# Optimization experiments

Hardware: AMD Instinct MI355X
Metric: run time of the kernel (lower is better)

Reference implementation:

```python
import jax, jax.numpy as jnp
import numpy as np

N = 16384      # nodes (radar cells x batched graphs)
H = 128        # n_hidden
N_ENV = 7
N_IN = N_ENV + 2 + 1  # env + coords + density = 10
T_CTX = 24
HORIZON = 40
T = T_CTX + HORIZON


def setup_inputs() -> dict:
    key = jax.random.key(0)
    ks = jax.random.split(key, 40)

    def w(k, shape, fan_in):
        return jax.random.normal(k, shape, jnp.float32) * np.float32(1.0 / np.sqrt(fan_in))

    inp = {}
    inp["x"] = jax.random.normal(ks[0], (N, T), jnp.float32)
    inp["coords"] = jax.random.normal(ks[1], (N, 2), jnp.float32)
    inp["env"] = jax.random.normal(ks[2], (N, N_ENV, T), jnp.float32)
    # --- encoder params ---
    inp["enc_W_in"] = w(ks[3], (H, N_IN), N_IN)           # Linear(n_in->H), no bias
    inp["enc_Wih0"] = w(ks[4], (4 * H, H), H)
    inp["enc_Whh0"] = w(ks[5], (4 * H, H), H)
    inp["enc_bih0"] = jnp.zeros((4 * H,), jnp.float32)
    inp["enc_bhh0"] = jnp.zeros((4 * H,), jnp.float32)
    inp["enc_Wih1"] = w(ks[6], (4 * H, H), H)
    inp["enc_Whh1"] = w(ks[7], (4 * H, H), H)
    inp["enc_bih1"] = jnp.zeros((4 * H,), jnp.float32)
    inp["enc_bhh1"] = jnp.zeros((4 * H,), jnp.float32)
    # --- NodeLSTM params ---
    inp["node_W_in"] = w(ks[8], (H, N_IN), N_IN)          # Linear(n_in->H), no bias
    inp["in_Wih"] = w(ks[9], (4 * H, 2 * H), 2 * H)       # lstm_in takes [inputs, enc_state]
    inp["in_Whh"] = w(ks[10], (4 * H, H), H)
    inp["in_bih"] = jnp.zeros((4 * H,), jnp.float32)
    inp["in_bhh"] = jnp.zeros((4 * H,), jnp.float32)
    inp["l1_Wih"] = w(ks[11], (4 * H, H), H)
    inp["l1_Whh"] = w(ks[12], (4 * H, H), H)
    inp["l1_bih"] = jnp.zeros((4 * H,), jnp.float32)
    inp["l1_bhh"] = jnp.zeros((4 * H,), jnp.float32)
    # hidden2in / hidden2out heads: Linear(H,H) -> ReLU -> Linear(H,1)
    inp["h2in_W1"] = w(ks[13], (H, H), H)
    inp["h2in_b1"] = jnp.zeros((H,), jnp.float32)
    inp["h2in_W2"] = w(ks[14], (1, H), H)
    inp["h2in_b2"] = jnp.zeros((1,), jnp.float32)
    inp["h2out_W1"] = w(ks[15], (H, H), H)
    inp["h2out_b1"] = jnp.zeros((H,), jnp.float32)
    inp["h2out_W2"] = w(ks[16], (1, H), H)
    inp["h2out_b2"] = jnp.zeros((1,), jnp.float32)
    return inp


def _lstm_cell(xin, h, c, Wih, Whh, bih, bhh):
    # torch.nn.LSTMCell semantics; gate order i, f, g, o
    gates = xin @ Wih.T + h @ Whh.T + (bih + bhh)
    i, f, g, o = jnp.split(gates, 4, axis=1)
    c_new = jax.nn.sigmoid(f) * c + jax.nn.sigmoid(i) * jnp.tanh(g)
    h_new = jax.nn.sigmoid(o) * jnp.tanh(c_new)
    return h_new, c_new


def reference(x, coords, env,
              enc_W_in, enc_Wih0, enc_Whh0, enc_bih0, enc_bhh0,
              enc_Wih1, enc_Whh1, enc_bih1, enc_bhh1,
              node_W_in, in_Wih, in_Whh, in_bih, in_bhh,
              l1_Wih, l1_Whh, l1_bih, l1_bhh,
              h2in_W1, h2in_b1, h2in_W2, h2in_b2,
              h2out_W1, h2out_b1, h2out_W2, h2out_b2):
    n = x.shape[0]
    z = jnp.zeros((n, H), x.dtype)

    # ---------- encoder: scan over T_CTX context steps ----------
    def enc_step(carry, xs):
        h0, c0, h1, c1 = carry
        xt, et = xs  # [N], [N, N_ENV]
        inp = jnp.concatenate([xt[:, None], coords, et], axis=1) @ enc_W_in.T
        h0, c0 = _lstm_cell(inp, h0, c0, enc_Wih0, enc_Whh0, enc_bih0, enc_bhh0)
        h1, c1 = _lstm_cell(h0, h1, c1, enc_Wih1, enc_Whh1, enc_bih1, enc_bhh1)
        return (h0, c0, h1, c1), None

    enc_xs = (x[:, :T_CTX].T, jnp.moveaxis(env[:, :, :T_CTX], 2, 0))
    (h0, c0, h1, c1), _ = jax.lax.scan(enc_step, (z, z, z, z), enc_xs)
    enc_state = h1  # h[-1] captured at setup_states, fixed over the horizon

    def head(hid, W1, b1, W2, b2):
        return jax.nn.sigmoid(jax.nn.relu(hid @ W1.T + b1) @ W2.T + b2)

    # ---------- decoder: scan over HORIZON forecast steps ----------
    def dec_step(carry, et):
        xc, h0, c0, h1, c1 = carry
        inp = jnp.concatenate([xc, coords, et], axis=1) @ node_W_in.T
        inp = jnp.concatenate([inp, enc_state], axis=1)  # [N, 2H]
        h0, c0 = _lstm_cell(inp, h0, c0, in_Wih, in_Whh, in_bih, in_bhh)
        h1, c1 = _lstm_cell(h0, h1, c1, l1_Wih, l1_Whh, l1_bih, l1_bhh)
        x_in = head(h1, h2in_W1, h2in_b1, h2in_W2, h2in_b2)
        x_out = head(h1, h2out_W1, h2out_b1, h2out_W2, h2out_b2)
        xn = xc + x_in - x_out * xc  # source/sink update, [N, 1]
        return (xn, h0, c0, h1, c1), xn

    x0 = x[:, T_CTX - 1][:, None]
    dec_xs = jnp.moveaxis(env[:, :, T_CTX:T_CTX + HORIZON], 2, 0)
    _, ys = jax.lax.scan(dec_step, (x0, h0, c0, h1, c1), dec_xs)  # [HORIZON, N, 1]
    return jnp.transpose(ys[..., 0], (1, 0))  # [N, HORIZON]
```

## Files before the change

### kernel.cpp

```cpp
#include <hip/hip_runtime.h>
#include <hip/hip_bf16.h>
#include <cstdint>
#include <cstddef>

typedef __bf16 bf16_t;
typedef bf16_t bf16x8 __attribute__((ext_vector_type(8)));
typedef bf16_t bf16x4 __attribute__((ext_vector_type(4)));
typedef float  f32x4  __attribute__((ext_vector_type(4)));

#define TT    64
#define T_CTX 24
#define HOR   40
#define SA    264
#define NTH   512

#define MFMA __builtin_amdgcn_mfma_f32_16x16x32_bf16

#define O_PKE   16
#define O_PKD   (O_PKE + 262144)
#define O_PKX   (O_PKD + 294912)
#define O_BIAS  (O_PKX + 131072)
#define O_HEADP (O_BIAS + 2048)
#define O_WINE  (O_HEADP + 512)
#define O_WINN  (O_WINE + 1536)
#define O_B2    (O_WINN + 1536)

struct Ptrs { const void* q[29]; };

__device__ __forceinline__ float sigm(float x) {
  return __builtin_amdgcn_rcpf(1.f + __expf(-x));
}
__device__ __forceinline__ float tanh_(float x) {
  return 1.f - 2.f * __builtin_amdgcn_rcpf(1.f + __expf(2.f * x));
}
__device__ __forceinline__ unsigned pk2(float a, float b) {
  unsigned ua = __float_as_uint(a), ub = __float_as_uint(b);
  ua = (ua + 0x7fffu + ((ua >> 16) & 1u)) >> 16;
  ub = (ub + 0x7fffu + ((ub >> 16) & 1u)) >> 16;
  return ua | (ub << 16);
}
__device__ __forceinline__ float uplo(unsigned p){ return __uint_as_float(p << 16); }
__device__ __forceinline__ float uphi(unsigned p){ return __uint_as_float(p & 0xffff0000u); }

__global__ void detect_kernel(const unsigned short* __restrict__ wsrc, int* __restrict__ flag)
{
  int tid = threadIdx.x;
  int wild = 0;
  for (int i = tid; i < 256; i += 64) {
    unsigned short b = wsrc[i];
    float v  = __uint_as_float(((unsigned)b) << 16);
    float av = fabsf(v);
    unsigned e = (b >> 7) & 0xff;
    if (av > 1000.f || e == 0xff || (((b & 0x7fff) != 0) && av < 1e-9f)) wild++;
  }
  for (int off = 32; off; off >>= 1) wild += __shfl_down(wild, off, 64);
  if (tid == 0) flag[0] = (wild > 16) ? 1 : 0;
}

__global__ void prep_kernel(Ptrs P, bf16_t* __restrict__ wb, const int* __restrict__ flag)
{
  const bool f32 = (flag[0] != 0);
  const int gtid = blockIdx.x * blockDim.x + threadIdx.x;
  const int gsz  = gridDim.x * blockDim.x;
  auto rd = [&](const void* src, int i) -> float {
    return f32 ? ((const float*)src)[i] : (float)((const bf16_t*)src)[i];
  };

  for (int i = gtid; i < 262144; i += gsz) {
    int w = i >> 15, r = i & 32767, f = r >> 9, e = r & 511;
    int ln = e >> 3, j = e & 7;
    int seg = f >> 5, fk = f & 31, kt = fk >> 2, g = fk & 3;
    int row = g * 128 + w * 16 + (ln & 15);
    int col = kt * 32 + ((ln >> 4) << 3) + j;
    float v;
    if (seg == 0) v = (col < 128) ? rd(P.q[4], row * 128 + col) : rd(P.q[5], row * 128 + col - 128);
    else          v = (col < 128) ? rd(P.q[8], row * 128 + col) : rd(P.q[9], row * 128 + col - 128);
    wb[O_PKE + i] = (bf16_t)v;
  }
  for (int i = gtid; i < 294912; i += gsz) {
    int w = i / 36864, r = i - w * 36864, f = r >> 9, e = r & 511;
    int ln = e >> 3, j = e & 7;
    int colk = ((ln >> 4) << 3) + j;
    float v;
    if (f < 64) {
      int seg = f >> 5, fk = f & 31, kt = fk >> 2, g = fk & 3;
      int row = g * 128 + w * 16 + (ln & 15);
      int col = kt * 32 + colk;
      if (seg == 0) v = (col < 128) ? rd(P.q[13], row * 256 + col) : rd(P.q[14], row * 128 + col - 128);
      else          v = (col < 128) ? rd(P.q[17], row * 128 + col) : rd(P.q[18], row * 128 + col - 128);
    } else {
      int f2 = f - 64, h = f2 >> 2, kt = f2 & 3;
      int row = w * 16 + (ln & 15);
      int col = kt * 32 + colk;
      v = rd(h ? P.q[25] : P.q[21], row * 128 + col);
    }
    wb[O_PKD + i] = (bf16_t)v;
  }
  for (int i = gtid; i < 131072; i += gsz) {
    int w = i >> 14, r = i & 16383, f = r >> 9, e = r & 511;
    int ln = e >> 3, j = e & 7;
    int kt = f >> 2, g = f & 3;
    int row = g * 128 + w * 16 + (ln & 15);
    int col = kt * 32 + ((ln >> 4) << 3) + j;
    wb[O_PKX + i] = (bf16_t)rd(P.q[13], row * 256 + 128 + col);
  }
  for (int i = gtid; i < 512; i += gsz) {
    wb[O_BIAS + i]        = (bf16_t)(rd(P.q[6],  i) + rd(P.q[7],  i));
    wb[O_BIAS + 512 + i]  = (bf16_t)(rd(P.q[10], i) + rd(P.q[11], i));
    wb[O_BIAS + 1024 + i] = (bf16_t)(rd(P.q[15], i) + rd(P.q[16], i));
    wb[O_BIAS + 1536 + i] = (bf16_t)(rd(P.q[19], i) + rd(P.q[20], i));
  }
  for (int i = gtid; i < 128; i += gsz) {
    wb[O_HEADP + i]       = (bf16_t)rd(P.q[22], i);
    wb[O_HEADP + 128 + i] = (bf16_t)rd(P.q[23], i);
    wb[O_HEADP + 256 + i] = (bf16_t)rd(P.q[26], i);
    wb[O_HEADP + 384 + i] = (bf16_t)rd(P.q[27], i);
  }
  for (int i = gtid; i < 1536; i += gsz) {
    int cc = i / 12, j = i % 12;
    wb[O_WINE + i] = (j < 10) ? (bf16_t)rd(P.q[3],  cc * 10 + j) : (bf16_t)0.f;
    wb[O_WINN + i] = (j < 10) ? (bf16_t)rd(P.q[12], cc * 10 + j) : (bf16_t)0.f;
  }
  if (gtid == 0) {
    wb[O_B2]     = (bf16_t)rd(P.q[24], 0);
    wb[O_B2 + 1] = (bf16_t)rd(P.q[28], 0);
  }
}

struct PreB { bf16x8 b[2][4]; };

__device__ __forceinline__ PreB preB(const bf16_t* __restrict__ pl) {
  PreB r;
#pragma unroll
  for (int p = 0; p < 2; ++p)
#pragma unroll
    for (int g = 0; g < 4; ++g)
      r.b[p][g] = *(const bf16x8*)(pl + (p * 4 + g) * 512);
  return r;
}

template<int NKT>
__device__ __forceinline__ void gemm_pk(f32x4 (&acc)[4][4], const bf16_t* __restrict__ As,
                                        const bf16_t* __restrict__ pl, const PreB& pre,
                                        int l, int q)
{
  bf16x8 bw[3][4];
#pragma unroll
  for (int g = 0; g < 4; ++g) { bw[0][g] = pre.b[0][g]; bw[1][g] = pre.b[1][g]; }
#pragma unroll
  for (int kt = 0; kt < NKT; ++kt) {
    bf16x8 a[4];
#pragma unroll
    for (int mt = 0; mt < 4; ++mt)
      a[mt] = *(const bf16x8*)(As + (mt * 16 + l) * SA + kt * 32 + q * 8);
    if (kt + 2 < NKT) {
#pragma unroll
      for (int g = 0; g < 4; ++g)
        bw[(kt + 2) % 3][g] = *(const bf16x8*)(pl + ((kt + 2) * 4 + g) * 512);
    }
#pragma unroll
    for (int g = 0; g < 4; ++g) {
      bf16x8 b = bw[kt % 3][g];
      acc[g][0] = MFMA(a[0], b, acc[g][0], 0, 0, 0);
      acc[g][1] = MFMA(a[1], b, acc[g][1], 0, 0, 0);
      acc[g][2] = MFMA(a[2], b, acc[g][2], 0, 0, 0);
      acc[g][3] = MFMA(a[3], b, acc[g][3], 0, 0, 0);
    }
  }
}

template<bool DUAL>
__device__ __forceinline__ void cell_up(f32x4 (&acc)[4][4], float (&c)[16],
                                        bf16_t* __restrict__ shb, bf16_t* __restrict__ sha,
                                        const bf16_t* __restrict__ bias,
                                        int wid, int l, int q)
{
  const int jc = wid * 16 + l;
  const float bi  = (float)bias[jc];
  const float bf_ = (float)bias[128 + jc];
  const float bg  = (float)bias[256 + jc];
  const float bo  = (float)bias[384 + jc];
#pragma unroll
  for (int mt = 0; mt < 4; ++mt) {
#pragma unroll
    for (int r = 0; r < 4; ++r) {
      float gi = acc[0][mt][r] + bi;
      float gf = acc[1][mt][r] + bf_;
      float gg = acc[2][mt][r] + bg;
      float go = acc[3][mt][r] + bo;
      float cn = sigm(gf) * c[mt * 4 + r] + sigm(gi) * tanh_(gg);
      float hh = sigm(go) * tanh_(cn);
      c[mt * 4 + r] = cn;
      const int row = mt * 16 + q * 4 + r;
      shb[row * SA + jc] = (bf16_t)hh;
      if (DUAL) sha[row * SA + jc] = (bf16_t)hh;
    }
  }
}

__device__ __forceinline__ void proj16(const float* v, const bf16_t* __restrict__ wbase,
                                       bf16_t* __restrict__ sx, int nd, int sub)
{
  bf16x8 o0, o1;
#pragma unroll
  for (int cc = 0; cc < 16; ++cc) {
    const bf16_t* wr = wbase + (sub * 16 + cc) * 12;
    bf16x4 w0 = *(const bf16x4*)(wr);
    bf16x4 w1 = *(const bf16x4*)(wr + 4);
    bf16x4 w2 = *(const bf16x4*)(wr + 8);
    float a = v[0] * (float)w0[0] + v[1] * (float)w0[1] + v[2] * (float)w0[2] + v[3] * (float)w0[3]
            + v[4] * (float)w1[0] + v[5] * (float)w1[1] + v[6] * (float)w1[2] + v[7] * (float)w1[3]
            + v[8] * (float)w2[0] + v[9] * (float)w2[1];
    if (cc < 8) o0[cc] = (bf16_t)a; else o1[cc - 8] = (bf16_t)a;
  }
  *(bf16x8*)(sx + nd * SA + sub * 16)     = o0;
  *(bf16x8*)(sx + nd * SA + sub * 16 + 8) = o1;
}

template<typename T>
__global__ __launch_bounds__(NTH, 2) void lstm_persist(
    const T* __restrict__ x, const T* __restrict__ coords, const T* __restrict__ env,
    const bf16_t* __restrict__ w, const int* __restrict__ flag, T* __restrict__ out)
{
  const bool want_f32 = (sizeof(T) == 4);
  if ((flag[0] != 0) != want_f32) return;

  __shared__ __align__(16) bf16_t bufA[64 * SA];
  __shared__ __align__(16) bf16_t bufB[64 * SA];
  __shared__ __align__(16) bf16_t s_win[2 * 128 * 12];
  __shared__ __align__(16) bf16_t s_bias[4 * 512];
  __shared__ float s_red[128];
  __shared__ float s_xc[64];

  const int tid  = threadIdx.x;
  const int wid  = tid >> 6;
  const int lane = tid & 63;
  const int l    = tid & 15;
  const int q    = (tid & 63) >> 4;
  const int node0 = blockIdx.x * 64;
  const int nd  = tid >> 3;
  const int sub = tid & 7;

  const bf16_t* plE0 = w + O_PKE + wid * 32768 + lane * 8;
  const bf16_t* plE1 = plE0 + 16384;
  const bf16_t* plD0 = w + O_PKD + wid * 36864 + lane * 8;
  const bf16_t* plD1 = plD0 + 16384;
  const bf16_t* plH  = plD0 + 32768;
  const bf16_t* plX  = w + O_PKX + wid * 16384 + lane * 8;

  for (int i = tid; i < 2048; i += NTH) s_bias[i] = w[O_BIAS + i];
  for (int i = tid; i < 3072; i += NTH) s_win[i]  = w[O_WINE + i];
  for (int i = tid; i < 64 * SA; i += NTH) { bufA[i] = (bf16_t)0.f; bufB[i] = (bf16_t)0.f; }

  const float cx = (float)coords[(size_t)(node0 + nd) * 2 + 0];
  const float cy = (float)coords[(size_t)(node0 + nd) * 2 + 1];

  float c0[16], c1[16];
#pragma unroll
  for (int i = 0; i < 16; ++i) { c0[i] = 0.f; c1[i] = 0.f; }

  PreB pA = preB(plE0);
  __syncthreads();

#pragma unroll 1
  for (int t = 0; t < T_CTX; ++t) {
    float v[10];
    v[0] = (float)x[(size_t)(node0 + nd) * TT + t];
    v[1] = cx; v[2] = cy;
#pragma unroll
    for (int e = 0; e < 7; ++e)
      v[3 + e] = (float)env[((size_t)(node0 + nd) * 7 + e) * TT + t];
    proj16(v, s_win, bufA, nd, sub);
    __syncthreads();

    f32x4 acc[4][4];
#pragma unroll
    for (int g = 0; g < 4; ++g)
#pragma unroll
      for (int mt = 0; mt < 4; ++mt) acc[g][mt] = f32x4{0.f, 0.f, 0.f, 0.f};
    gemm_pk<8>(acc, bufA, plE0, pA, l, q);
    PreB pC = preB(plE1);
    __syncthreads();
    cell_up<true>(acc, c0, bufB, bufA + 128, s_bias, wid, l, q);
    __syncthreads();

#pragma unroll
    for (int g = 0; g < 4; ++g)
#pragma unroll
      for (int mt = 0; mt < 4; ++mt) acc[g][mt] = f32x4{0.f, 0.f, 0.f, 0.f};
    gemm_pk<8>(acc, bufB, plE1, pC, l, q);
    pA = preB((t < T_CTX - 1) ? plE0 : plX);
    __syncthreads();
    cell_up<false>(acc, c1, bufB + 128, nullptr, s_bias + 512, wid, l, q);
  }
  __syncthreads();

  uint2 geh[4][4];
  {
    f32x4 acc[4][4];
#pragma unroll
    for (int g = 0; g < 4; ++g)
#pragma unroll
      for (int mt = 0; mt < 4; ++mt) acc[g][mt] = f32x4{0.f, 0.f, 0.f, 0.f};
    gemm_pk<4>(acc, bufB + 128, plX, pA, l, q);
#pragma unroll
    for (int g = 0; g < 4; ++g)
#pragma unroll
      for (int mt = 0; mt < 4; ++mt)
        geh[g][mt] = uint2{pk2(acc[g][mt][0], acc[g][mt][1]),
                           pk2(acc[g][mt][2], acc[g][mt][3])};
  }
  if (tid < 64) s_xc[tid] = (float)x[(size_t)(node0 + tid) * TT + (T_CTX - 1)];
  const float b2i = (float)w[O_B2];
  const float b2o = (float)w[O_B2 + 1];
  const float b1i = (float)w[O_HEADP + wid * 16 + l];
  const float w2i = (float)w[O_HEADP + 128 + wid * 16 + l];
  const float b1o = (float)w[O_HEADP + 256 + wid * 16 + l];
  const float w2o = (float)w[O_HEADP + 384 + wid * 16 + l];
  pA = preB(plD0);
  __syncthreads();

#pragma unroll 1
  for (int s = 0; s < HOR; ++s) {
    const int t = T_CTX + s;
    float v[10];
    v[0] = s_xc[nd];
    v[1] = cx; v[2] = cy;
#pragma unroll
    for (int e = 0; e < 7; ++e)
      v[3 + e] = (float)env[((size_t)(node0 + nd) * 7 + e) * TT + t];
    proj16(v, s_win + 1536, bufA, nd, sub);
    __syncthreads();

    f32x4 acc[4][4];
#pragma unroll
    for (int g = 0; g < 4; ++g)
#pragma unroll
      for (int mt = 0; mt < 4; ++mt)
        acc[g][mt] = f32x4{uplo(geh[g][mt].x), uphi(geh[g][mt].x),
                           uplo(geh[g][mt].y), uphi(geh[g][mt].y)};
    gemm_pk<8>(acc, bufA, plD0, pA, l, q);
    PreB pC = preB(plD1);
    __syncthreads();
    cell_up<true>(acc, c0, bufB, bufA + 128, s_bias + 1024, wid, l, q);
    __syncthreads();

#pragma unroll
    for (int g = 0; g < 4; ++g)
#pragma unroll
      for (int mt = 0; mt < 4; ++mt) acc[g][mt] = f32x4{0.f, 0.f, 0.f, 0.f};
    gemm_pk<8>(acc, bufB, plD1, pC, l, q);
    bf16x8 hb[8];
#pragma unroll
    for (int f = 0; f < 8; ++f) hb[f] = *(const bf16x8*)(plH + f * 512);
    __syncthreads();
    cell_up<false>(acc, c1, bufB + 128, nullptr, s_bias + 1536, wid, l, q);
    if (tid < 128) s_red[tid] = 0.f;
    pA = preB(plD0);
    __syncthreads();

    f32x4 hacc[2][4];
#pragma unroll
    for (int hd = 0; hd < 2; ++hd)
#pragma unroll
      for (int mt = 0; mt < 4; ++mt) hacc[hd][mt] = f32x4{0.f, 0.f, 0.f, 0.f};
#pragma unroll
    for (int kt = 0; kt < 4; ++kt) {
      bf16x8 a[4];
#pragma unroll
      for (int mt = 0; mt < 4; ++mt)
        a[mt] = *(const bf16x8*)(bufB + 128 + (mt * 16 + l) * SA + kt * 32 + q * 8);
#pragma unroll
      for (int mt = 0; mt < 4; ++mt) {
        hacc[0][mt] = MFMA(a[mt], hb[kt],     hacc[0][mt], 0, 0, 0);
        hacc[1][mt] = MFMA(a[mt], hb[4 + kt], hacc[1][mt], 0, 0, 0);
      }
    }
#pragma unroll
    for (int hd = 0; hd < 2; ++hd) {
      const float b1v = hd ? b1o : b1i;
      const float w2v = hd ? w2o : w2i;
#pragma unroll
      for (int mt = 0; mt < 4; ++mt)
#pragma unroll
        for (int r = 0; r < 4; ++r) {
          float val = fmaxf(hacc[hd][mt][r] + b1v, 0.f) * w2v;
          val += __shfl_xor(val, 1, 64);
          val += __shfl_xor(val, 2, 64);
          val += __shfl_xor(val, 4, 64);
          val += __shfl_xor(val, 8, 64);
          if (l == 0) atomicAdd(&s_red[hd * 64 + mt * 16 + q * 4 + r], val);
        }
    }
    __syncthreads();
    if (tid < 64) {
      float xc = s_xc[tid];
      float si = sigm(s_red[tid] + b2i);
      float so = sigm(s_red[64 + tid] + b2o);
      float xn = xc + si - so * xc;
      s_xc[tid] = xn;
      out[(size_t)(node0 + tid) * HOR + s] = (T)xn;
    }
    __syncthreads();
  }
}

extern "C" void kernel_launch(void* const* d_in, const int* in_sizes, int n_in,
                              void* d_out, int out_size, void* d_ws, size_t ws_size,
                              hipStream_t stream) {
  (void)in_sizes; (void)n_in; (void)out_size; (void)ws_size;
  Ptrs P;
  for (int i = 0; i < 29; ++i) P.q[i] = d_in[i];
  int*    flag = (int*)d_ws;
  bf16_t* w    = (bf16_t*)d_ws;

  detect_kernel<<<1, 64, 0, stream>>>((const unsigned short*)d_in[4], flag);
  prep_kernel<<<256, 256, 0, stream>>>(P, w, flag);
  lstm_persist<float><<<256, NTH, 0, stream>>>(
      (const float*)d_in[0], (const float*)d_in[1], (const float*)d_in[2],
      w, flag, (float*)d_out);
  lstm_persist<bf16_t><<<256, NTH, 0, stream>>>(
      (const bf16_t*)d_in[0], (const bf16_t*)d_in[1], (const bf16_t*)d_in[2],
      w, flag, (bf16_t*)d_out);
}
```

Before: 2.159 ms.

## Deepen weight prefetch window, double-buffer env loads in LDS, batch output stores

The B-operand prefetch window in the packed GEMM grows from 2 k-tiles to 5, issuing each refill after the MFMAs that consume the slot. Per-step env and x loads are spread across all threads as non-temporal loads, fetched one timestep ahead, and staged in a double-buffered shared array. Outputs are collected in LDS and written once at the end with coalesced non-temporal stores. The larger prefetch window raises VGPR pressure, which with launch bounds of 2 blocks per CU could cause spills. The extra shared buffers also add LDS usage.

```diff
diff --git a/kernel.cpp b/kernel.cpp
--- a/kernel.cpp
+++ b/kernel.cpp
@@ -13,6 +13,7 @@
 #define HOR   40
 #define SA    264
 #define NTH   512
+#define WIN   5
 
 #define MFMA __builtin_amdgcn_mfma_f32_16x16x32_bf16
 
@@ -41,6 +42,14 @@
 }
 __device__ __forceinline__ float uplo(unsigned p){ return __uint_as_float(p << 16); }
 __device__ __forceinline__ float uphi(unsigned p){ return __uint_as_float(p & 0xffff0000u); }
+
+__device__ __forceinline__ float ldnt(const float* p) {
+  return __builtin_nontemporal_load(p);
+}
+__device__ __forceinline__ float ldnt(const bf16_t* p) {
+  unsigned short u = __builtin_nontemporal_load((const unsigned short*)p);
+  return __uint_as_float(((unsigned)u) << 16);
+}
 
 __global__ void detect_kernel(const unsigned short* __restrict__ wsrc, int* __restrict__ flag)
 {
@@ -127,12 +136,12 @@
   }
 }
 
-struct PreB { bf16x8 b[2][4]; };
+struct PreB { bf16x8 b[WIN][4]; };
 
 __device__ __forceinline__ PreB preB(const bf16_t* __restrict__ pl) {
   PreB r;
 #pragma unroll
-  for (int p = 0; p < 2; ++p)
+  for (int p = 0; p < WIN; ++p)
 #pragma unroll
     for (int g = 0; g < 4; ++g)
       r.b[p][g] = *(const bf16x8*)(pl + (p * 4 + g) * 512);
@@ -141,30 +150,27 @@
 
 template<int NKT>
 __device__ __forceinline__ void gemm_pk(f32x4 (&acc)[4][4], const bf16_t* __restrict__ As,
-                                        const bf16_t* __restrict__ pl, const PreB& pre,
+                                        const bf16_t* __restrict__ pl, PreB pre,
                                         int l, int q)
 {
-  bf16x8 bw[3][4];
-#pragma unroll
-  for (int g = 0; g < 4; ++g) { bw[0][g] = pre.b[0][g]; bw[1][g] = pre.b[1][g]; }
 #pragma unroll
   for (int kt = 0; kt < NKT; ++kt) {
     bf16x8 a[4];
 #pragma unroll
     for (int mt = 0; mt < 4; ++mt)
       a[mt] = *(const bf16x8*)(As + (mt * 16 + l) * SA + kt * 32 + q * 8);
-    if (kt + 2 < NKT) {
-#pragma unroll
-      for (int g = 0; g < 4; ++g)
-        bw[(kt + 2) % 3][g] = *(const bf16x8*)(pl + ((kt + 2) * 4 + g) * 512);
-    }
 #pragma unroll
     for (int g = 0; g < 4; ++g) {
-      bf16x8 b = bw[kt % 3][g];
+      bf16x8 b = pre.b[kt % WIN][g];
       acc[g][0] = MFMA(a[0], b, acc[g][0], 0, 0, 0);
       acc[g][1] = MFMA(a[1], b, acc[g][1], 0, 0, 0);
       acc[g][2] = MFMA(a[2], b, acc[g][2], 0, 0, 0);
       acc[g][3] = MFMA(a[3], b, acc[g][3], 0, 0, 0);
+    }
+    if (kt + WIN < NKT) {
+#pragma unroll
+      for (int g = 0; g < 4; ++g)
+        pre.b[kt % WIN][g] = *(const bf16x8*)(pl + ((kt + WIN) * 4 + g) * 512);
     }
   }
 }
@@ -231,6 +237,8 @@
   __shared__ __align__(16) bf16_t s_bias[4 * 512];
   __shared__ float s_red[128];
   __shared__ float s_xc[64];
+  __shared__ float s_env[2][64][8];
+  __shared__ float s_out[64 * 40];
 
   const int tid  = threadIdx.x;
   const int wid  = tid >> 6;
@@ -240,6 +248,8 @@
   const int node0 = blockIdx.x * 64;
   const int nd  = tid >> 3;
   const int sub = tid & 7;
+  const int nd_e = tid / 7;
+  const int e_e  = tid - nd_e * 7;
 
   const bf16_t* plE0 = w + O_PKE + wid * 32768 + lane * 8;
   const bf16_t* plE1 = plE0 + 16384;
@@ -252,8 +262,11 @@
   for (int i = tid; i < 3072; i += NTH) s_win[i]  = w[O_WINE + i];
   for (int i = tid; i < 64 * SA; i += NTH) { bufA[i] = (bf16_t)0.f; bufB[i] = (bf16_t)0.f; }
 
-  const float cx = (float)coords[(size_t)(node0 + nd) * 2 + 0];
-  const float cy = (float)coords[(size_t)(node0 + nd) * 2 + 1];
+  if (tid < 448) s_env[0][nd_e][e_e] = ldnt(&env[(size_t)((node0 + nd_e) * 7 + e_e) * TT]);
+  else           s_env[0][tid - 448][7] = ldnt(&x[(size_t)(node0 + tid - 448) * TT]);
+
+  const float cx = ldnt(&coords[(size_t)(node0 + nd) * 2 + 0]);
+  const float cy = ldnt(&coords[(size_t)(node0 + nd) * 2 + 1]);
 
   float c0[16], c1[16];
 #pragma unroll
@@ -264,13 +277,20 @@
 
 #pragma unroll 1
   for (int t = 0; t < T_CTX; ++t) {
+    const int tn = t + 1;
+    float tpre = 0.f;
+    if (tid < 448) tpre = ldnt(&env[(size_t)((node0 + nd_e) * 7 + e_e) * TT + tn]);
+    else           tpre = ldnt(&x[(size_t)(node0 + tid - 448) * TT + tn]);
+
     float v[10];
-    v[0] = (float)x[(size_t)(node0 + nd) * TT + t];
+    v[0] = s_env[t & 1][nd][7];
     v[1] = cx; v[2] = cy;
 #pragma unroll
-    for (int e = 0; e < 7; ++e)
-      v[3 + e] = (float)env[((size_t)(node0 + nd) * 7 + e) * TT + t];
+    for (int e = 0; e < 7; ++e) v[3 + e] = s_env[t & 1][nd][e];
     proj16(v, s_win, bufA, nd, sub);
+
+    if (tid < 448) s_env[tn & 1][nd_e][e_e] = tpre;
+    else           s_env[tn & 1][tid - 448][7] = tpre;
     __syncthreads();
 
     f32x4 acc[4][4];
@@ -310,26 +330,37 @@
         geh[g][mt] = uint2{pk2(acc[g][mt][0], acc[g][mt][1]),
                            pk2(acc[g][mt][2], acc[g][mt][3])};
   }
-  if (tid < 64) s_xc[tid] = (float)x[(size_t)(node0 + tid) * TT + (T_CTX - 1)];
+  if (tid < 64) s_xc[tid] = ldnt(&x[(size_t)(node0 + tid) * TT + (T_CTX - 1)]);
   const float b2i = (float)w[O_B2];
   const float b2o = (float)w[O_B2 + 1];
   const float b1i = (float)w[O_HEADP + wid * 16 + l];
   const float w2i = (float)w[O_HEADP + 128 + wid * 16 + l];
   const float b1o = (float)w[O_HEADP + 256 + wid * 16 + l];
   const float w2o = (float)w[O_HEADP + 384 + wid * 16 + l];
-  pA = preB(plD0);
+  PreB pD = preB(plD0);
   __syncthreads();
 
 #pragma unroll 1
   for (int s = 0; s < HOR; ++s) {
     const int t = T_CTX + s;
+    const int tn = t + 1;
+    float tpre = 0.f;
+    if (tn < TT) {
+      if (tid < 448) tpre = ldnt(&env[(size_t)((node0 + nd_e) * 7 + e_e) * TT + tn]);
+      else           tpre = ldnt(&x[(size_t)(node0 + tid - 448) * TT + tn]);
+    }
+
     float v[10];
     v[0] = s_xc[nd];
     v[1] = cx; v[2] = cy;
 #pragma unroll
-    for (int e = 0; e < 7; ++e)
-      v[3 + e] = (float)env[((size_t)(node0 + nd) * 7 + e) * TT + t];
+    for (int e = 0; e < 7; ++e) v[3 + e] = s_env[t & 1][nd][e];
     proj16(v, s_win + 1536, bufA, nd, sub);
+
+    if (tn < TT) {
+      if (tid < 448) s_env[tn & 1][nd_e][e_e] = tpre;
+      else           s_env[tn & 1][tid - 448][7] = tpre;
+    }
     __syncthreads();
 
     f32x4 acc[4][4];
@@ -339,7 +370,7 @@
       for (int mt = 0; mt < 4; ++mt)
         acc[g][mt] = f32x4{uplo(geh[g][mt].x), uphi(geh[g][mt].x),
                            uplo(geh[g][mt].y), uphi(geh[g][mt].y)};
-    gemm_pk<8>(acc, bufA, plD0, pA, l, q);
+    gemm_pk<8>(acc, bufA, plD0, pD, l, q);
     PreB pC = preB(plD1);
     __syncthreads();
     cell_up<true>(acc, c0, bufB, bufA + 128, s_bias + 1024, wid, l, q);
@@ -356,7 +387,7 @@
     __syncthreads();
     cell_up<false>(acc, c1, bufB + 128, nullptr, s_bias + 1536, wid, l, q);
     if (tid < 128) s_red[tid] = 0.f;
-    pA = preB(plD0);
+    pD = preB(plD0);
     __syncthreads();
 
     f32x4 hacc[2][4];
@@ -399,9 +430,21 @@
       float so = sigm(s_red[64 + tid] + b2o);
       float xn = xc + si - so * xc;
       s_xc[tid] = xn;
-      out[(size_t)(node0 + tid) * HOR + s] = (T)xn;
-    }
-    __syncthreads();
+      s_out[tid * 40 + s] = xn;
+    }
+    __syncthreads();
+  }
+
+  for (int i = tid; i < 64 * 40; i += NTH) {
+    float vv = s_out[i];
+    if constexpr (sizeof(T) == 4) {
+      __builtin_nontemporal_store(vv, (float*)out + (size_t)node0 * HOR + i);
+    } else {
+      bf16_t bv = (bf16_t)vv;
+      unsigned short us;
+      __builtin_memcpy(&us, &bv, 2);
+      __builtin_nontemporal_store(us, (unsigned short*)out + (size_t)node0 * HOR + i);
+    }
   }
 }
 
```

New measurement: 2.473 ms. 14.5% more time.
